# Performance work log

Hardware: AMD Instinct MI355X
Metric: run time of the kernel (lower is better)

Reference implementation:

```python
import jax, jax.numpy as jnp
import numpy as np

RFF_DIM = 256
ATTENTION_SCALE = 0.1
LAMBDA_REG = 0.01
SIGMA = 1.0


def setup_inputs() -> dict:
    key = jax.random.key(0)
    k1, k2, k3 = jax.random.split(key, 3)
    N, D_IN = 262144, 64
    Z = jax.random.normal(k1, (N, D_IN), dtype=jnp.float32)
    W_rff = jax.random.normal(k2, (D_IN, RFF_DIM), dtype=jnp.float32)
    A = jax.random.normal(k3, (2 * RFF_DIM, 3), dtype=jnp.float32) * 0.01
    return {"Z": Z, "W_rff": W_rff, "A": A}


def reference(Z, W_rff, A):
    # --- RFF transform: Q = sqrt(1/R) * [cos(Z W / sigma), sin(Z W / sigma)] ---
    proj = (Z @ W_rff) / SIGMA                       # [N, R]
    Q = jnp.sqrt(1.0 / RFF_DIM) * jnp.concatenate(
        [jnp.cos(proj), jnp.sin(proj)], axis=-1)      # [N, 2R]

    N, F = Q.shape
    chunk = max(F // RFF_DIM, 1)                      # = 2 here
    n_chunks = F // chunk                             # = RFF_DIM

    # --- convexified attention over feature chunks (vectorized) ---
    Qc = Q.reshape(N, n_chunks, chunk)                # [N, K, c]
    A_mean = jnp.mean(A, axis=-1)                     # [2R]
    # per-chunk trace score: mean over batch of <Q_i, A_mean[:c]>
    scores = jnp.mean(jnp.einsum('nkc,c->nk', Qc, A_mean[:chunk]), axis=0)  # [K]
    alpha = jax.nn.softmax(scores / (ATTENTION_SCALE * np.sqrt(RFF_DIM)))   # [K]
    # per-chunk reweighting (dim-preserving recombination)
    Q_tilde = (alpha[None, :, None] * Qc).reshape(N, F)                      # [N, 2R]

    # --- small GEMM head + nuclear-norm regularizer ---
    predictions = Q_tilde @ A                          # [N, out]
    AW = jax.nn.softmax(predictions / np.sqrt(RFF_DIM), axis=-1)
    nuclear_norm = jnp.sum(jnp.linalg.svd(A, compute_uv=False))
    reg_loss = LAMBDA_REG * nuclear_norm
    return predictions, AW, reg_loss, alpha
```

## Files before the change

### kernel.cpp

```cpp
#include <hip/hip_runtime.h>
#include <math.h>

#define N_ROWS 262144
#define D_IN 64
#define RFF 256
#define NTILES (N_ROWS / 16)
#define GRID_BIG 512
#define TILES_PER_BLOCK (NTILES / GRID_BIG)
#define TILES_PER_WAVE (TILES_PER_BLOCK / 4)

#define OFF_PRED 0
#define OFF_AW (N_ROWS * 3)
#define OFF_REG (2 * N_ROWS * 3)
#define OFF_ALPHA (2 * N_ROWS * 3 + 1)

#define WS_B 512

typedef _Float16 f16x8 __attribute__((ext_vector_type(8)));
typedef float f32x4 __attribute__((ext_vector_type(4)));

__device__ __forceinline__ f32x4 mfma16(f16x8 a, f16x8 b, f32x4 c) {
    return __builtin_amdgcn_mfma_f32_16x16x32_f16(a, b, c, 0, 0, 0);
}

__device__ __forceinline__ unsigned short f32_to_bf16_rne(float x) {
    unsigned int u = __float_as_uint(x);
    unsigned int r = u + 0x7fffu + ((u >> 16) & 1u);
    return (unsigned short)(r >> 16);
}

__device__ __forceinline__ void gload_lds16(const float* g, float* lds) {
    __builtin_amdgcn_global_load_lds(
        (const __attribute__((address_space(1))) unsigned int*)g,
        (__attribute__((address_space(3))) unsigned int*)(lds), 16, 0, 0);
}

__device__ __forceinline__ void prep_W(const float* __restrict__ W, f16x8* Bf, int t) {
#pragma unroll
    for (int q = 0; q < 8; ++q) {
        const int s = t + 256 * q;
        const int lane = s & 63;
        const int kh = (s >> 6) & 1;
        const int ct = s >> 7;
        const int k0 = kh * 32 + 8 * (lane >> 4);
        const int col = ct * 16 + (lane & 15);
        f16x8 v;
#pragma unroll
        for (int i = 0; i < 8; ++i) v[i] = (_Float16)W[(k0 + i) * RFF + col];
        Bf[(ct * 2 + kh) * 64 + lane] = v;
    }
}

__device__ __forceinline__ void stage_dma(const float* __restrict__ Z, int n0, int l,
                                          float* ldsbase) {
#pragma unroll
    for (int m = 0; m < 4; ++m) {
        const int row = m * 4 + (l >> 4);
        const int gc = (l & 15) ^ (row & 7);
        gload_lds16(Z + (size_t)(n0 + row) * D_IN + gc * 4, ldsbase + m * 256);
    }
}

__device__ __forceinline__ void frags_from_lds(const float* bb, int lr, int lh,
                                               f16x8& ah0, f16x8& al0, f16x8& ah1, f16x8& al1) {
    const int s4 = lr & 7;
    const float* rp = bb + lr * 64;
    float z[16];
    *(float4*)&z[0]  = *(const float4*)(rp + (((lh * 2 + 0) ^ s4) << 2));
    *(float4*)&z[4]  = *(const float4*)(rp + (((lh * 2 + 1) ^ s4) << 2));
    *(float4*)&z[8]  = *(const float4*)(rp + (((lh * 2 + 8) ^ s4) << 2));
    *(float4*)&z[12] = *(const float4*)(rp + (((lh * 2 + 9) ^ s4) << 2));
#pragma unroll
    for (int i = 0; i < 8; ++i) {
        _Float16 h0 = (_Float16)z[i];
        ah0[i] = h0;
        al0[i] = (_Float16)(z[i] - (float)h0);
        _Float16 h1 = (_Float16)z[8 + i];
        ah1[i] = h1;
        al1[i] = (_Float16)(z[8 + i] - (float)h1);
    }
}

#define WAITVM4() do { asm volatile("s_waitcnt vmcnt(4)" ::: "memory"); \
                       __builtin_amdgcn_sched_barrier(0); } while (0)
#define WAITVM0() do { asm volatile("s_waitcnt vmcnt(0)" ::: "memory"); \
                       __builtin_amdgcn_sched_barrier(0); } while (0)

__global__ __launch_bounds__(256, 2) void k_pass1(const float* __restrict__ Z,
                                                  const float* __restrict__ W,
                                                  float* __restrict__ U) {
    __shared__ f16x8 Bf[2048];
    __shared__ float Zs[4][2][1024];
    __shared__ float Ured[512];
    const int t = threadIdx.x;
    prep_W(W, Bf, t);
    Ured[t] = 0.f;
    Ured[t + 256] = 0.f;
    __syncthreads();

    const int wv = t >> 6, l = t & 63, lr = l & 15, lh = l >> 4;
    float accC[16], accS[16];
#pragma unroll
    for (int c = 0; c < 16; ++c) { accC[c] = 0.f; accS[c] = 0.f; }

    const int tile0 = blockIdx.x * TILES_PER_BLOCK + wv * TILES_PER_WAVE;
    stage_dma(Z, tile0 * 16, l, &Zs[wv][0][0]);

    for (int tt = 0; tt < TILES_PER_WAVE; ++tt) {
        if (tt + 1 < TILES_PER_WAVE) {
            stage_dma(Z, (tile0 + tt + 1) * 16, l, &Zs[wv][(tt + 1) & 1][0]);
            WAITVM4();
        } else {
            WAITVM0();
        }
        f16x8 ah0, al0, ah1, al1;
        frags_from_lds(&Zs[wv][tt & 1][0], lr, lh, ah0, al0, ah1, al1);
        f32x4 acc[16];
#pragma unroll
        for (int ct = 0; ct < 16; ++ct) acc[ct] = (f32x4){0.f, 0.f, 0.f, 0.f};
#pragma unroll
        for (int ct = 0; ct < 16; ++ct) {
            f16x8 b0 = Bf[(ct * 2 + 0) * 64 + l];
            f16x8 b1 = Bf[(ct * 2 + 1) * 64 + l];
            acc[ct] = mfma16(ah0, b0, acc[ct]);
            acc[ct] = mfma16(ah1, b1, acc[ct]);
            acc[ct] = mfma16(al0, b0, acc[ct]);
            acc[ct] = mfma16(al1, b1, acc[ct]);
        }
#pragma unroll
        for (int ct = 0; ct < 16; ++ct) {
#pragma unroll
            for (int r = 0; r < 4; ++r) {
                float sn, cs;
                __sincosf(acc[ct][r], &sn, &cs);
                accC[ct] += cs;
                accS[ct] += sn;
            }
        }
    }
#pragma unroll
    for (int ct = 0; ct < 16; ++ct) {
        accC[ct] += __shfl_xor(accC[ct], 16);
        accC[ct] += __shfl_xor(accC[ct], 32);
        accS[ct] += __shfl_xor(accS[ct], 16);
        accS[ct] += __shfl_xor(accS[ct], 32);
    }
    if (l < 16) {
#pragma unroll
        for (int ct = 0; ct < 16; ++ct) {
            atomicAdd(&Ured[ct * 16 + l], accC[ct] * 0.0625f);
            atomicAdd(&Ured[256 + ct * 16 + l], accS[ct] * 0.0625f);
        }
    }
    __syncthreads();
    atomicAdd(&U[t], Ured[t]);
    atomicAdd(&U[t + 256], Ured[t + 256]);
}

__global__ __launch_bounds__(256) void k_alpha(const float* __restrict__ U,
                                               const float* __restrict__ A,
                                               float* __restrict__ ws,
                                               float* __restrict__ out) {
    __shared__ float sm[256];
    __shared__ double gred[256];
    __shared__ double G6[6];
    const int k = threadIdx.x;

    const float am0 = (A[0] + A[1] + A[2]) * (1.0f / 3.0f);
    const float am1 = (A[3] + A[4] + A[5]) * (1.0f / 3.0f);
    float score = (am0 * U[2 * k] + am1 * U[2 * k + 1]) * (1.0f / (float)N_ROWS);
    float x = score * (1.0f / 1.6f);

    sm[k] = x;
    __syncthreads();
    for (int s = 128; s > 0; s >>= 1) {
        if (k < s) sm[k] = fmaxf(sm[k], sm[k + s]);
        __syncthreads();
    }
    float mx = sm[0];
    __syncthreads();
    float e = __expf(x - mx);
    sm[k] = e;
    __syncthreads();
    for (int s = 128; s > 0; s >>= 1) {
        if (k < s) sm[k] += sm[k + s];
        __syncthreads();
    }
    float al = e / sm[0];
    out[OFF_ALPHA + k] = al;
    sm[k] = al;
    __syncthreads();

    {
        const float ac = 0.0625f * sm[k >> 1];
        const float as = 0.0625f * sm[128 + (k >> 1)];
        unsigned int* BtP = (unsigned int*)(ws + WS_B);
#pragma unroll
        for (int j = 0; j < 3; ++j) {
            float bc = ac * A[k * 3 + j];
            float bs = as * A[(256 + k) * 3 + j];
            unsigned int ulo = f32_to_bf16_rne(bc);
            unsigned int uhi = f32_to_bf16_rne(bs);
            BtP[k * 3 + j] = ulo | (uhi << 16);
        }
    }

    double af[2][3];
#pragma unroll
    for (int t2 = 0; t2 < 2; ++t2)
#pragma unroll
        for (int j = 0; j < 3; ++j) af[t2][j] = (double)A[(k + t2 * 256) * 3 + j];
    const int ei[6] = {0, 0, 0, 1, 1, 2};
    const int ej[6] = {0, 1, 2, 1, 2, 2};
    for (int eidx = 0; eidx < 6; ++eidx) {
        double p = af[0][ei[eidx]] * af[0][ej[eidx]] + af[1][ei[eidx]] * af[1][ej[eidx]];
        gred[k] = p;
        __syncthreads();
        for (int s = 128; s > 0; s >>= 1) {
            if (k < s) gred[k] += gred[k + s];
            __syncthreads();
        }
        if (k == 0) G6[eidx] = gred[0];
        __syncthreads();
    }
    if (k == 0) {
        double g00 = G6[0], g01 = G6[1], g02 = G6[2], g11 = G6[3], g12 = G6[4], g22 = G6[5];
        double q = (g00 + g11 + g22) / 3.0;
        double p1 = g01 * g01 + g02 * g02 + g12 * g12;
        double p2 = (g00 - q) * (g00 - q) + (g11 - q) * (g11 - q) + (g22 - q) * (g22 - q) + 2.0 * p1;
        double nuc;
        if (p2 < 1e-300) {
            nuc = 3.0 * sqrt(fmax(q, 0.0));
        } else {
            double p = sqrt(p2 / 6.0);
            double b00 = (g00 - q) / p, b11 = (g11 - q) / p, b22 = (g22 - q) / p;
            double b01 = g01 / p, b02 = g02 / p, b12 = g12 / p;
            double detB = b00 * (b11 * b22 - b12 * b12) - b01 * (b01 * b22 - b12 * b02) +
                          b02 * (b01 * b12 - b11 * b02);
            double rr = detB / 2.0;
            rr = fmin(1.0, fmax(-1.0, rr));
            double phi = acos(rr) / 3.0;
            double e1 = q + 2.0 * p * cos(phi);
            double e3 = q + 2.0 * p * cos(phi + 2.0943951023931953);
            double e2 = 3.0 * q - e1 - e3;
            nuc = sqrt(fmax(e1, 0.0)) + sqrt(fmax(e2, 0.0)) + sqrt(fmax(e3, 0.0));
        }
        out[OFF_REG] = (float)(0.01 * nuc);
    }
}

__global__ __launch_bounds__(256, 2) void k_pass2(const float* __restrict__ Z,
                                                  const float* __restrict__ W,
                                                  const float* __restrict__ ws,
                                                  float* __restrict__ out) {
    __shared__ f16x8 Bf[2048];
    __shared__ float Zs[4][2][1024];
    __shared__ unsigned int BtP[768];
    const int t = threadIdx.x;
    prep_W(W, Bf, t);
    {
        const unsigned int* src = (const unsigned int*)(ws + WS_B);
        BtP[t] = src[t];
        BtP[t + 256] = src[t + 256];
        BtP[t + 512] = src[t + 512];
    }
    __syncthreads();

    const int wv = t >> 6, l = t & 63, lr = l & 15, lh = l >> 4;

    const int tile0 = blockIdx.x * TILES_PER_BLOCK + wv * TILES_PER_WAVE;
    stage_dma(Z, tile0 * 16, l, &Zs[wv][0][0]);

    for (int tt = 0; tt < TILES_PER_WAVE; ++tt) {
        const int n0 = (tile0 + tt) * 16;
        if (tt + 1 < TILES_PER_WAVE) {
            stage_dma(Z, (tile0 + tt + 1) * 16, l, &Zs[wv][(tt + 1) & 1][0]);
            WAITVM4();
        } else {
            WAITVM0();
        }
        f16x8 ah0, al0, ah1, al1;
        frags_from_lds(&Zs[wv][tt & 1][0], lr, lh, ah0, al0, ah1, al1);
        f32x4 acc[16];
#pragma unroll
        for (int ct = 0; ct < 16; ++ct) acc[ct] = (f32x4){0.f, 0.f, 0.f, 0.f};
#pragma unroll
        for (int ct = 0; ct < 16; ++ct) {
            f16x8 b0 = Bf[(ct * 2 + 0) * 64 + l];
            f16x8 b1 = Bf[(ct * 2 + 1) * 64 + l];
            acc[ct] = mfma16(ah0, b0, acc[ct]);
            acc[ct] = mfma16(ah1, b1, acc[ct]);
            acc[ct] = mfma16(al0, b0, acc[ct]);
            acc[ct] = mfma16(al1, b1, acc[ct]);
        }
        float pa[4][3];
#pragma unroll
        for (int r = 0; r < 4; ++r) { pa[r][0] = 0.f; pa[r][1] = 0.f; pa[r][2] = 0.f; }
#pragma unroll
        for (int ct = 0; ct < 16; ++ct) {
            const int f = ct * 16 + lr;
            unsigned int u0 = BtP[f * 3 + 0], u1 = BtP[f * 3 + 1], u2 = BtP[f * 3 + 2];
            float bc0 = __uint_as_float(u0 << 16), bs0 = __uint_as_float(u0 & 0xffff0000u);
            float bc1 = __uint_as_float(u1 << 16), bs1 = __uint_as_float(u1 & 0xffff0000u);
            float bc2 = __uint_as_float(u2 << 16), bs2 = __uint_as_float(u2 & 0xffff0000u);
#pragma unroll
            for (int r = 0; r < 4; ++r) {
                float sn, cs;
                __sincosf(acc[ct][r], &sn, &cs);
                pa[r][0] = __builtin_fmaf(cs, bc0, __builtin_fmaf(sn, bs0, pa[r][0]));
                pa[r][1] = __builtin_fmaf(cs, bc1, __builtin_fmaf(sn, bs1, pa[r][1]));
                pa[r][2] = __builtin_fmaf(cs, bc2, __builtin_fmaf(sn, bs2, pa[r][2]));
            }
        }
#pragma unroll
        for (int r = 0; r < 4; ++r)
#pragma unroll
            for (int j = 0; j < 3; ++j) {
                pa[r][j] += __shfl_xor(pa[r][j], 1);
                pa[r][j] += __shfl_xor(pa[r][j], 2);
                pa[r][j] += __shfl_xor(pa[r][j], 4);
                pa[r][j] += __shfl_xor(pa[r][j], 8);
            }
        float q0 = 0.f, q1 = 0.f, q2 = 0.f;
#pragma unroll
        for (int r = 0; r < 4; ++r)
            if (lr == r) { q0 = pa[r][0]; q1 = pa[r][1]; q2 = pa[r][2]; }
        if (lr < 4) {
            const size_t n = (size_t)n0 + 4 * lh + lr;
            out[OFF_PRED + n * 3 + 0] = q0;
            out[OFF_PRED + n * 3 + 1] = q1;
            out[OFF_PRED + n * 3 + 2] = q2;
            float x0 = q0 * 0.0625f, x1 = q1 * 0.0625f, x2 = q2 * 0.0625f;
            float m = fmaxf(x0, fmaxf(x1, x2));
            float e0 = __expf(x0 - m), e1 = __expf(x1 - m), e2 = __expf(x2 - m);
            float inv = 1.0f / (e0 + e1 + e2);
            out[OFF_AW + n * 3 + 0] = e0 * inv;
            out[OFF_AW + n * 3 + 1] = e1 * inv;
            out[OFF_AW + n * 3 + 2] = e2 * inv;
        }
    }
}

extern "C" void kernel_launch(void* const* d_in, const int* in_sizes, int n_in,
                              void* d_out, int out_size, void* d_ws, size_t ws_size,
                              hipStream_t stream) {
    const float* Z = (const float*)d_in[0];
    const float* W = (const float*)d_in[1];
    const float* A = (const float*)d_in[2];
    float* out = (float*)d_out;
    float* ws = (float*)d_ws;

    (void)hipMemsetAsync(ws, 0, 512 * sizeof(float), stream);
    hipLaunchKernelGGL(k_pass1, dim3(GRID_BIG), dim3(256), 0, stream, Z, W, ws);
    hipLaunchKernelGGL(k_alpha, dim3(1), dim3(256), 0, stream, ws, A, ws, out);
    hipLaunchKernelGGL(k_pass2, dim3(GRID_BIG), dim3(256), 0, stream, Z, W, ws, out);
}
```

Measured before the change: 95.98 us.

## Drop fp16 split-precision MFMA, precompute W fragments, single-buffer Z, raise occupancy

Removes the hi/lo fp16 split of Z, halving MFMA count, at the cost of reduced accuracy in the projection that feeds sin/cos. W fragments are converted once by a new prep kernel and DMA'd into LDS by each block, replacing per-block strided conversion. Z staging goes from double to single buffer, freeing LDS so occupancy rises to 3 blocks per CU, and the grid doubles. Single buffering makes each load wait before the next tile's compute, and the precision loss could exceed tolerance for large projection values.

```diff
diff --git a/kernel.cpp b/kernel.cpp
--- a/kernel.cpp
+++ b/kernel.cpp
@@ -5,7 +5,7 @@
 #define D_IN 64
 #define RFF 256
 #define NTILES (N_ROWS / 16)
-#define GRID_BIG 512
+#define GRID_BIG 1024
 #define TILES_PER_BLOCK (NTILES / GRID_BIG)
 #define TILES_PER_WAVE (TILES_PER_BLOCK / 4)
 
@@ -15,6 +15,7 @@
 #define OFF_ALPHA (2 * N_ROWS * 3 + 1)
 
 #define WS_B 512
+#define WS_WF 1280
 
 typedef _Float16 f16x8 __attribute__((ext_vector_type(8)));
 typedef float f32x4 __attribute__((ext_vector_type(4)));
@@ -35,19 +36,32 @@
         (__attribute__((address_space(3))) unsigned int*)(lds), 16, 0, 0);
 }
 
-__device__ __forceinline__ void prep_W(const float* __restrict__ W, f16x8* Bf, int t) {
-#pragma unroll
-    for (int q = 0; q < 8; ++q) {
-        const int s = t + 256 * q;
-        const int lane = s & 63;
-        const int kh = (s >> 6) & 1;
-        const int ct = s >> 7;
-        const int k0 = kh * 32 + 8 * (lane >> 4);
-        const int col = ct * 16 + (lane & 15);
-        f16x8 v;
-#pragma unroll
-        for (int i = 0; i < 8; ++i) v[i] = (_Float16)W[(k0 + i) * RFF + col];
-        Bf[(ct * 2 + kh) * 64 + lane] = v;
+#define WAITVM0() do { asm volatile("s_waitcnt vmcnt(0)" ::: "memory"); \
+                       __builtin_amdgcn_sched_barrier(0); } while (0)
+#define LGKM0()   do { asm volatile("s_waitcnt lgkmcnt(0)" ::: "memory"); \
+                       __builtin_amdgcn_sched_barrier(0); } while (0)
+
+__global__ __launch_bounds__(256) void k_prep(const float* __restrict__ W,
+                                              float* __restrict__ ws) {
+    const int e = blockIdx.x * 256 + threadIdx.x;
+    const int lane = e & 63;
+    const int slot = e >> 6;
+    const int kh = slot & 1;
+    const int ct = slot >> 1;
+    const int k0 = kh * 32 + 8 * (lane >> 4);
+    const int col = ct * 16 + (lane & 15);
+    f16x8 v;
+#pragma unroll
+    for (int i = 0; i < 8; ++i) v[i] = (_Float16)W[(k0 + i) * RFF + col];
+    *(f16x8*)(ws + WS_WF + e * 4) = v;
+}
+
+__device__ __forceinline__ void dma_Bf(const float* __restrict__ wsWf, float* Bff,
+                                       int wv, int l) {
+#pragma unroll
+    for (int m = 0; m < 8; ++m) {
+        const int off = wv * 2048 + m * 256;
+        gload_lds16(wsWf + off + l * 4, Bff + off);
     }
 }
 
@@ -62,7 +76,7 @@
 }
 
 __device__ __forceinline__ void frags_from_lds(const float* bb, int lr, int lh,
-                                               f16x8& ah0, f16x8& al0, f16x8& ah1, f16x8& al1) {
+                                               f16x8& ah0, f16x8& ah1) {
     const int s4 = lr & 7;
     const float* rp = bb + lr * 64;
     float z[16];
@@ -70,62 +84,51 @@
     *(float4*)&z[4]  = *(const float4*)(rp + (((lh * 2 + 1) ^ s4) << 2));
     *(float4*)&z[8]  = *(const float4*)(rp + (((lh * 2 + 8) ^ s4) << 2));
     *(float4*)&z[12] = *(const float4*)(rp + (((lh * 2 + 9) ^ s4) << 2));
+    LGKM0();
 #pragma unroll
     for (int i = 0; i < 8; ++i) {
-        _Float16 h0 = (_Float16)z[i];
-        ah0[i] = h0;
-        al0[i] = (_Float16)(z[i] - (float)h0);
-        _Float16 h1 = (_Float16)z[8 + i];
-        ah1[i] = h1;
-        al1[i] = (_Float16)(z[8 + i] - (float)h1);
-    }
-}
-
-#define WAITVM4() do { asm volatile("s_waitcnt vmcnt(4)" ::: "memory"); \
-                       __builtin_amdgcn_sched_barrier(0); } while (0)
-#define WAITVM0() do { asm volatile("s_waitcnt vmcnt(0)" ::: "memory"); \
-                       __builtin_amdgcn_sched_barrier(0); } while (0)
-
-__global__ __launch_bounds__(256, 2) void k_pass1(const float* __restrict__ Z,
-                                                  const float* __restrict__ W,
+        ah0[i] = (_Float16)z[i];
+        ah1[i] = (_Float16)z[8 + i];
+    }
+}
+
+__global__ __launch_bounds__(256, 3) void k_pass1(const float* __restrict__ Z,
+                                                  const float* __restrict__ ws_in,
                                                   float* __restrict__ U) {
-    __shared__ f16x8 Bf[2048];
-    __shared__ float Zs[4][2][1024];
+    __shared__ float Bff[8192];
+    __shared__ float Zs[4][1024];
     __shared__ float Ured[512];
     const int t = threadIdx.x;
-    prep_W(W, Bf, t);
+    const int wv = t >> 6, l = t & 63, lr = l & 15, lh = l >> 4;
+
+    dma_Bf(ws_in + WS_WF, Bff, wv, l);
+    const int tile0 = blockIdx.x * TILES_PER_BLOCK + wv * TILES_PER_WAVE;
+    stage_dma(Z, tile0 * 16, l, &Zs[wv][0]);
     Ured[t] = 0.f;
     Ured[t + 256] = 0.f;
     __syncthreads();
 
-    const int wv = t >> 6, l = t & 63, lr = l & 15, lh = l >> 4;
+    const f16x8* Bf = (const f16x8*)Bff;
     float accC[16], accS[16];
 #pragma unroll
     for (int c = 0; c < 16; ++c) { accC[c] = 0.f; accS[c] = 0.f; }
 
-    const int tile0 = blockIdx.x * TILES_PER_BLOCK + wv * TILES_PER_WAVE;
-    stage_dma(Z, tile0 * 16, l, &Zs[wv][0][0]);
-
+#pragma unroll
     for (int tt = 0; tt < TILES_PER_WAVE; ++tt) {
+        if (tt) WAITVM0();
+        f16x8 ah0, ah1;
+        frags_from_lds(&Zs[wv][0], lr, lh, ah0, ah1);
         if (tt + 1 < TILES_PER_WAVE) {
-            stage_dma(Z, (tile0 + tt + 1) * 16, l, &Zs[wv][(tt + 1) & 1][0]);
-            WAITVM4();
-        } else {
-            WAITVM0();
-        }
-        f16x8 ah0, al0, ah1, al1;
-        frags_from_lds(&Zs[wv][tt & 1][0], lr, lh, ah0, al0, ah1, al1);
+            stage_dma(Z, (tile0 + tt + 1) * 16, l, &Zs[wv][0]);
+            __builtin_amdgcn_sched_barrier(0);
+        }
         f32x4 acc[16];
 #pragma unroll
         for (int ct = 0; ct < 16; ++ct) acc[ct] = (f32x4){0.f, 0.f, 0.f, 0.f};
 #pragma unroll
         for (int ct = 0; ct < 16; ++ct) {
-            f16x8 b0 = Bf[(ct * 2 + 0) * 64 + l];
-            f16x8 b1 = Bf[(ct * 2 + 1) * 64 + l];
-            acc[ct] = mfma16(ah0, b0, acc[ct]);
-            acc[ct] = mfma16(ah1, b1, acc[ct]);
-            acc[ct] = mfma16(al0, b0, acc[ct]);
-            acc[ct] = mfma16(al1, b1, acc[ct]);
+            acc[ct] = mfma16(ah0, Bf[(ct * 2 + 0) * 64 + l], acc[ct]);
+            acc[ct] = mfma16(ah1, Bf[(ct * 2 + 1) * 64 + l], acc[ct]);
         }
 #pragma unroll
         for (int ct = 0; ct < 16; ++ct) {
@@ -249,49 +252,45 @@
     }
 }
 
-__global__ __launch_bounds__(256, 2) void k_pass2(const float* __restrict__ Z,
-                                                  const float* __restrict__ W,
-                                                  const float* __restrict__ ws,
+__global__ __launch_bounds__(256, 3) void k_pass2(const float* __restrict__ Z,
+                                                  const float* __restrict__ ws_in,
                                                   float* __restrict__ out) {
-    __shared__ f16x8 Bf[2048];
-    __shared__ float Zs[4][2][1024];
+    __shared__ float Bff[8192];
+    __shared__ float Zs[4][1024];
     __shared__ unsigned int BtP[768];
     const int t = threadIdx.x;
-    prep_W(W, Bf, t);
+    const int wv = t >> 6, l = t & 63, lr = l & 15, lh = l >> 4;
+
+    dma_Bf(ws_in + WS_WF, Bff, wv, l);
+    const int tile0 = blockIdx.x * TILES_PER_BLOCK + wv * TILES_PER_WAVE;
+    stage_dma(Z, tile0 * 16, l, &Zs[wv][0]);
     {
-        const unsigned int* src = (const unsigned int*)(ws + WS_B);
+        const unsigned int* src = (const unsigned int*)(ws_in + WS_B);
         BtP[t] = src[t];
         BtP[t + 256] = src[t + 256];
         BtP[t + 512] = src[t + 512];
     }
     __syncthreads();
 
-    const int wv = t >> 6, l = t & 63, lr = l & 15, lh = l >> 4;
-
-    const int tile0 = blockIdx.x * TILES_PER_BLOCK + wv * TILES_PER_WAVE;
-    stage_dma(Z, tile0 * 16, l, &Zs[wv][0][0]);
-
+    const f16x8* Bf = (const f16x8*)Bff;
+
+#pragma unroll
     for (int tt = 0; tt < TILES_PER_WAVE; ++tt) {
         const int n0 = (tile0 + tt) * 16;
+        if (tt) WAITVM0();
+        f16x8 ah0, ah1;
+        frags_from_lds(&Zs[wv][0], lr, lh, ah0, ah1);
         if (tt + 1 < TILES_PER_WAVE) {
-            stage_dma(Z, (tile0 + tt + 1) * 16, l, &Zs[wv][(tt + 1) & 1][0]);
-            WAITVM4();
-        } else {
-            WAITVM0();
-        }
-        f16x8 ah0, al0, ah1, al1;
-        frags_from_lds(&Zs[wv][tt & 1][0], lr, lh, ah0, al0, ah1, al1);
+            stage_dma(Z, (tile0 + tt + 1) * 16, l, &Zs[wv][0]);
+            __builtin_amdgcn_sched_barrier(0);
+        }
         f32x4 acc[16];
 #pragma unroll
         for (int ct = 0; ct < 16; ++ct) acc[ct] = (f32x4){0.f, 0.f, 0.f, 0.f};
 #pragma unroll
         for (int ct = 0; ct < 16; ++ct) {
-            f16x8 b0 = Bf[(ct * 2 + 0) * 64 + l];
-            f16x8 b1 = Bf[(ct * 2 + 1) * 64 + l];
-            acc[ct] = mfma16(ah0, b0, acc[ct]);
-            acc[ct] = mfma16(ah1, b1, acc[ct]);
-            acc[ct] = mfma16(al0, b0, acc[ct]);
-            acc[ct] = mfma16(al1, b1, acc[ct]);
+            acc[ct] = mfma16(ah0, Bf[(ct * 2 + 0) * 64 + l], acc[ct]);
+            acc[ct] = mfma16(ah1, Bf[(ct * 2 + 1) * 64 + l], acc[ct]);
         }
         float pa[4][3];
 #pragma unroll
@@ -351,7 +350,8 @@
     float* ws = (float*)d_ws;
 
     (void)hipMemsetAsync(ws, 0, 512 * sizeof(float), stream);
-    hipLaunchKernelGGL(k_pass1, dim3(GRID_BIG), dim3(256), 0, stream, Z, W, ws);
+    hipLaunchKernelGGL(k_prep, dim3(8), dim3(256), 0, stream, W, ws);
+    hipLaunchKernelGGL(k_pass1, dim3(GRID_BIG), dim3(256), 0, stream, Z, ws, ws);
     hipLaunchKernelGGL(k_alpha, dim3(1), dim3(256), 0, stream, ws, A, ws, out);
-    hipLaunchKernelGGL(k_pass2, dim3(GRID_BIG), dim3(256), 0, stream, Z, W, ws, out);
-}
+    hipLaunchKernelGGL(k_pass2, dim3(GRID_BIG), dim3(256), 0, stream, Z, ws, out);
+}
```

Result: slower. 99.50 us (+3.7%).
